# Kernel tuning notes

Measured on AMD Instinct MI355X. Metric: run time of the kernel, lower is better.

The kernel has to match this reference:

```python
import jax, jax.numpy as jnp
import numpy as np

INPUT_DIM = 1024
OUTPUT_DIM = 1024
DEGREE = 8


def setup_inputs() -> dict:
    key = jax.random.key(0)
    k1, k2 = jax.random.split(key)
    x = jax.random.normal(k1, (8192, INPUT_DIM), dtype=jnp.float32)
    std = 1.0 / (INPUT_DIM * (DEGREE + 1))
    cheby_coeffs = jax.random.normal(k2, (INPUT_DIM, OUTPUT_DIM, DEGREE + 1), dtype=jnp.float32) * std
    return {"x": x, "cheby_coeffs": cheby_coeffs}


def reference(x, cheby_coeffs):
    # x: [B, I]; cheby_coeffs: [I, O, D+1]
    degree = cheby_coeffs.shape[-1] - 1
    t = jnp.clip(jnp.tanh(x), -0.999, 0.999)            # [B, I]
    theta = jnp.arccos(t)[..., None]                     # [B, I, 1]
    arange = jnp.arange(degree + 1, dtype=x.dtype)       # [D+1]
    basis = jnp.cos(theta * arange)                      # [B, I, D+1] Chebyshev T_d(t)
    y = jnp.einsum('bid,iod->bo', basis, cheby_coeffs)   # [B, O]
    return y
```

## Files before the change

kernel.cpp:

```cpp
#include <hip/hip_runtime.h>
#include <stdint.h>

#define B_ROWS 8192
#define I_DIM  1024
#define N_DIM  1024
#define NDEG   9
#define K_DIM  (I_DIM * (NDEG-1))

#define BM 256
#define BN 128
#define BK 64
#define NT (K_DIM / BK)

typedef __attribute__((ext_vector_type(8)))  short short8;
typedef __attribute__((ext_vector_type(16))) float f32x16;

__device__ __forceinline__ unsigned short f2bf(float f) {
  union { float f; uint32_t u; } v; v.f = f;
  uint32_t u = v.u;
  u += 0x7FFFu + ((u >> 16) & 1u);
  return (unsigned short)(u >> 16);
}

__device__ __forceinline__ float bf2f(unsigned short h) {
  union { uint32_t u; float f; } v; v.u = ((uint32_t)h) << 16;
  return v.f;
}

__device__ __forceinline__ uint32_t pk_bf16(float lo, float hi) {
  uint32_t r;
  asm("v_cvt_pk_bf16_f32 %0, %1, %2" : "=v"(r) : "v"(lo), "v"(hi));
  return r;
}

__device__ __forceinline__ float fast_tanh(float x) {
  float e = __expf(2.0f * x);
  return 1.0f - __fdividef(2.0f, e + 1.0f);
}

__global__ __launch_bounds__(256) void repack_kernel(const float* __restrict__ cf,
                                                     unsigned short* __restrict__ Bt2,
                                                     float* __restrict__ bias) {
  __shared__ unsigned short L[32][584];
  const int i0  = blockIdx.x * 32;
  const int o0  = blockIdx.y * 64;
  const int tid = threadIdx.x;

  #pragma unroll
  for (int j = 0; j < 18; ++j) {
    const int f4  = j * 256 + tid;
    const int il  = f4 / 144;
    const int odq = f4 % 144;
    const float4 v = *reinterpret_cast<const float4*>(
        cf + ((size_t)(i0 + il) * N_DIM + o0) * NDEG + (size_t)odq * 4);
    ushort4 w;
    w.x = f2bf(v.x); w.y = f2bf(v.y); w.z = f2bf(v.z); w.w = f2bf(v.w);
    *reinterpret_cast<ushort4*>(&L[il][odq * 4]) = w;
  }
  __syncthreads();

  const int o_rel = tid >> 2;
  const int ci    = tid & 3;
  const int o     = o0 + o_rel;
  const int ntb   = o >> 7;
  const int gb    = (o & 127) >> 5;
  const int r31   = o & 31;
  const int kti   = (i0 >> 3) + ci;
  const size_t base = (size_t)ntb * 1048576 + (size_t)kti * 8192 + (size_t)r31 * 8;
  #pragma unroll
  for (int p = 0; p < 8; ++p) {
    const int il = ci * 8 + p;
    uint4 u;
    u.x = (uint32_t)L[il][o_rel*9 + 1] | ((uint32_t)L[il][o_rel*9 + 2] << 16);
    u.y = (uint32_t)L[il][o_rel*9 + 3] | ((uint32_t)L[il][o_rel*9 + 4] << 16);
    u.z = (uint32_t)L[il][o_rel*9 + 5] | ((uint32_t)L[il][o_rel*9 + 6] << 16);
    u.w = (uint32_t)L[il][o_rel*9 + 7] | ((uint32_t)L[il][o_rel*9 + 8] << 16);
    *reinterpret_cast<uint4*>(Bt2 + base + (size_t)(gb * 8 + p) * 256) = u;
  }
  if (tid < 64) {
    float s = 0.f;
    #pragma unroll
    for (int il = 0; il < 32; ++il) s += bf2f(L[il][tid * 9]);
    atomicAdd(&bias[o0 + tid], s);
  }
}

__global__ __launch_bounds__(768, 3) void gemm_kernel(const float* __restrict__ x,
                                                      const unsigned short* __restrict__ Bt2,
                                                      const float* __restrict__ bias,
                                                      float* __restrict__ C) {
  extern __shared__ unsigned short sm[];
  const int tid  = threadIdx.x;
  const int wave = tid >> 6;

  const int bid = blockIdx.x;
  const int mt  = (bid & 7) + 8 * (bid >> 6);
  const int nt  = (bid >> 3) & 7;
  const int m0  = mt * BM;
  const int n0  = nt * BN;

  if (wave < 8) {
    const int lane = tid & 63;
    const int l31  = lane & 31;
    const int half = lane >> 5;
    const int wm   = wave >> 1;
    const int wn   = wave & 1;

    const int aoff0 = ((wm * 2 + 0) * 8 + half) * 256 + l31 * 8;
    const int aoff1 = ((wm * 2 + 1) * 8 + half) * 256 + l31 * 8;
    const int boff0 = ((wn * 2 + 0) * 8 + half) * 256 + l31 * 8;
    const int boff1 = ((wn * 2 + 1) * 8 + half) * 256 + l31 * 8;

    f32x16 acc[2][2];
    #pragma unroll
    for (int a = 0; a < 2; ++a)
      #pragma unroll
      for (int b = 0; b < 2; ++b)
        #pragma unroll
        for (int r = 0; r < 16; ++r)
          acc[a][b][r] = 0.f;

    short8 av[2][4], bv[2][4];

#define READ4(As_, Bs_, ks) {                                                                \
    av[0][ks] = *reinterpret_cast<const short8*>(&(As_)[aoff0 + (ks) * 512]);                \
    av[1][ks] = *reinterpret_cast<const short8*>(&(As_)[aoff1 + (ks) * 512]);                \
    bv[0][ks] = *reinterpret_cast<const short8*>(&(Bs_)[boff0 + (ks) * 512]);                \
    bv[1][ks] = *reinterpret_cast<const short8*>(&(Bs_)[boff1 + (ks) * 512]); }

#define MFMA4(ks)                                                                            \
    acc[0][0] = __builtin_amdgcn_mfma_f32_32x32x16_bf16(av[0][ks], bv[0][ks], acc[0][0], 0, 0, 0); \
    acc[0][1] = __builtin_amdgcn_mfma_f32_32x32x16_bf16(av[0][ks], bv[1][ks], acc[0][1], 0, 0, 0); \
    acc[1][0] = __builtin_amdgcn_mfma_f32_32x32x16_bf16(av[1][ks], bv[0][ks], acc[1][0], 0, 0, 0); \
    acc[1][1] = __builtin_amdgcn_mfma_f32_32x32x16_bf16(av[1][ks], bv[1][ks], acc[1][1], 0, 0, 0);

#define CPIN { __builtin_amdgcn_sched_group_barrier(0x100, 4, 0);                            \
               __builtin_amdgcn_sched_group_barrier(0x008, 4, 0); }

#define CTILE(bufsel) {                                                                      \
    const unsigned short* As_ = &sm[(bufsel) * 16384];                                       \
    const unsigned short* Bs_ = &sm[32768 + (bufsel) * 8192];                                \
    READ4(As_, Bs_, 0)                                                                       \
    READ4(As_, Bs_, 1) MFMA4(0) CPIN                                                         \
    READ4(As_, Bs_, 2) MFMA4(1) CPIN                                                         \
    READ4(As_, Bs_, 3) MFMA4(2) CPIN                                                         \
    MFMA4(3) __builtin_amdgcn_sched_group_barrier(0x008, 4, 0); }

#define CBAR { __builtin_amdgcn_sched_barrier(0); __builtin_amdgcn_s_barrier();              \
               __builtin_amdgcn_sched_barrier(0); }

    CBAR
    for (int kt = 0; kt < 126; kt += 2) {
      CTILE(0) CBAR
      CTILE(1) CBAR
    }
    CTILE(0) CBAR
    CTILE(1)
#undef CTILE
#undef CPIN
#undef READ4

    #pragma unroll
    for (int ni = 0; ni < 2; ++ni) {
      const int col  = n0 + wn * 64 + ni * 32 + l31;
      const float bc = bias[col];
      #pragma unroll
      for (int mi = 0; mi < 2; ++mi) {
        const int rbase = m0 + wm * 64 + mi * 32 + 4 * half;
        #pragma unroll
        for (int r = 0; r < 16; ++r) {
          const int row = rbase + (r & 3) + 8 * (r >> 2);
          C[(size_t)row * N_DIM + col] = acc[mi][ni][r] + bc;
        }
      }
    }
#undef MFMA4
#undef CBAR
  } else {
    const int pr = tid - 512;
    const float* xrow = x + (size_t)(m0 + pr) * I_DIM;
    const unsigned short* BtSlab = Bt2 + (size_t)nt * 1048576;
    const int awbase = (pr >> 5) * 2048 + (pr & 31) * 8;
    const int prw8   = pr * 8;

#define STAGEB(bufsel, kt1) {                                                                \
    _Pragma("unroll")                                                                        \
    for (int q = 0; q < 4; ++q) {                                                            \
      __builtin_amdgcn_global_load_lds(                                                      \
        (const __attribute__((address_space(1))) void*)(BtSlab + (size_t)(kt1) * 8192 + q * 2048 + prw8), \
        (__attribute__((address_space(3))) void*)&sm[32768 + (bufsel) * 8192 + q * 2048 + prw8], 16, 0, 0); \
    } }

#define BASIS8(bufsel, f0, f1) {                                                             \
    const float tin[8] = {(f0).x, (f0).y, (f0).z, (f0).w, (f1).x, (f1).y, (f1).z, (f1).w};   \
    _Pragma("unroll")                                                                        \
    for (int s = 0; s < 8; ++s) {                                                            \
      float t = fast_tanh(tin[s]);                                                           \
      t = fminf(fmaxf(t, -0.999f), 0.999f);                                                  \
      const float t2 = t + t;                                                                \
      const float T1 = t;                                                                    \
      const float T2 = t2 * t - 1.0f;                                                        \
      const float T3 = t2 * T2 - T1;                                                         \
      const float T4 = t2 * T3 - T2;                                                         \
      const float T5 = t2 * T4 - T3;                                                         \
      const float T6 = t2 * T5 - T4;                                                         \
      const float T7 = t2 * T6 - T5;                                                         \
      const float T8 = t2 * T7 - T6;                                                         \
      uint4 u;                                                                               \
      u.x = pk_bf16(T1, T2); u.y = pk_bf16(T3, T4);                                          \
      u.z = pk_bf16(T5, T6); u.w = pk_bf16(T7, T8);                                          \
      *reinterpret_cast<uint4*>(&sm[(bufsel) * 16384 + awbase + s * 256]) = u;               \
    } }

    float4 xE0, xE1, xO0, xO1;
    xE0 = *reinterpret_cast<const float4*>(xrow + 0);
    xE1 = *reinterpret_cast<const float4*>(xrow + 4);
    xO0 = *reinterpret_cast<const float4*>(xrow + 8);
    xO1 = *reinterpret_cast<const float4*>(xrow + 12);
    STAGEB(0, 0)
    BASIS8(0, xE0, xE1)
    __builtin_amdgcn_sched_barrier(0);
    asm volatile("s_waitcnt vmcnt(0) lgkmcnt(0)" ::: "memory");
    __builtin_amdgcn_s_barrier();
    __builtin_amdgcn_sched_barrier(0);

#define PTILE(kt_, XU0, XU1, XL0, XL1, LX) {                                                 \
    STAGEB(((kt_) + 1) & 1, (kt_) + 1)                                                       \
    __builtin_amdgcn_sched_barrier(0);                                                       \
    BASIS8(((kt_) + 1) & 1, XU0, XU1)                                                        \
    __builtin_amdgcn_sched_barrier(0);                                                       \
    if (LX) {                                                                                \
      XL0 = *reinterpret_cast<const float4*>(xrow + ((kt_) + 2) * 8);                        \
      XL1 = *reinterpret_cast<const float4*>(xrow + ((kt_) + 2) * 8 + 4);                    \
    }                                                                                        \
    __builtin_amdgcn_sched_barrier(0);                                                       \
    if (LX) { asm volatile("s_waitcnt vmcnt(2) lgkmcnt(0)" ::: "memory"); }                  \
    else    { asm volatile("s_waitcnt vmcnt(0) lgkmcnt(0)" ::: "memory"); }                  \
    __builtin_amdgcn_s_barrier();                                                            \
    __builtin_amdgcn_sched_barrier(0); }

    for (int kt = 0; kt < 126; kt += 2) {
      PTILE(kt,     xO0, xO1, xE0, xE1, 1)
      PTILE(kt + 1, xE0, xE1, xO0, xO1, 1)
    }
    PTILE(126, xO0, xO1, xE0, xE1, 0)
#undef PTILE
#undef BASIS8
#undef STAGEB
  }
}

extern "C" void kernel_launch(void* const* d_in, const int* in_sizes, int n_in,
                              void* d_out, int out_size, void* d_ws, size_t ws_size,
                              hipStream_t stream) {
  const float* x      = (const float*)d_in[0];
  const float* coeffs = (const float*)d_in[1];
  float* y            = (float*)d_out;

  const size_t bt_bytes = (size_t)N_DIM * K_DIM * sizeof(unsigned short);
  unsigned short* Bt2 = (unsigned short*)d_ws;
  float* bias         = (float*)((char*)d_ws + bt_bytes);

  hipMemsetAsync(bias, 0, N_DIM * sizeof(float), stream);

  hipFuncSetAttribute((const void*)gemm_kernel,
                      hipFuncAttributeMaxDynamicSharedMemorySize, 98304);

  repack_kernel<<<dim3(I_DIM / 32, N_DIM / 64), 256, 0, stream>>>(coeffs, Bt2, bias);
  gemm_kernel<<<(B_ROWS / BM) * (N_DIM / BN), 768, 98304, stream>>>(x, Bt2, bias, y);
}
```

Baseline: 266.3 us.

## Drop LDS staging; compute basis and load B directly into registers per wave

Removes the producer-wave specialization and shared-memory double buffering. Each MFMA wave now loads its own x scalars and B fragments straight from global memory into registers, computes the Chebyshev basis in registers and feeds the MFMAs, with software double-buffered register prefetch. This eliminates LDS traffic and block barriers, but each wave recomputes the basis for its rows (2x redundancy across wn) and issues scattered scalar and vector global loads that rely on cache for reuse.

```diff
diff --git a/kernel.cpp b/kernel.cpp
--- a/kernel.cpp
+++ b/kernel.cpp
@@ -85,13 +85,17 @@
   }
 }
 
-__global__ __launch_bounds__(768, 3) void gemm_kernel(const float* __restrict__ x,
-                                                      const unsigned short* __restrict__ Bt2,
-                                                      const float* __restrict__ bias,
-                                                      float* __restrict__ C) {
-  extern __shared__ unsigned short sm[];
+__global__ __launch_bounds__(512) void gemm_kernel(const float* __restrict__ x,
+                                                   const unsigned short* __restrict__ Bt2,
+                                                   const float* __restrict__ bias,
+                                                   float* __restrict__ C) {
   const int tid  = threadIdx.x;
+  const int lane = tid & 63;
   const int wave = tid >> 6;
+  const int l31  = lane & 31;
+  const int half = lane >> 5;
+  const int wm   = wave >> 1;
+  const int wn   = wave & 1;
 
   const int bid = blockIdx.x;
   const int mt  = (bid & 7) + 8 * (bid >> 6);
@@ -99,154 +103,95 @@
   const int m0  = mt * BM;
   const int n0  = nt * BN;
 
-  if (wave < 8) {
-    const int lane = tid & 63;
-    const int l31  = lane & 31;
-    const int half = lane >> 5;
-    const int wm   = wave >> 1;
-    const int wn   = wave & 1;
-
-    const int aoff0 = ((wm * 2 + 0) * 8 + half) * 256 + l31 * 8;
-    const int aoff1 = ((wm * 2 + 1) * 8 + half) * 256 + l31 * 8;
-    const int boff0 = ((wn * 2 + 0) * 8 + half) * 256 + l31 * 8;
-    const int boff1 = ((wn * 2 + 1) * 8 + half) * 256 + l31 * 8;
-
-    f32x16 acc[2][2];
+  const float* xb = x + (size_t)(m0 + wm * 64 + l31) * I_DIM + half;
+  const unsigned short* bf = Bt2 + (size_t)nt * 1048576 + (size_t)(wn * 16 + half) * 256 + l31 * 8;
+
+  f32x16 acc[2][2];
+  #pragma unroll
+  for (int a = 0; a < 2; ++a)
     #pragma unroll
-    for (int a = 0; a < 2; ++a)
+    for (int b = 0; b < 2; ++b)
       #pragma unroll
-      for (int b = 0; b < 2; ++b)
-        #pragma unroll
-        for (int r = 0; r < 16; ++r)
-          acc[a][b][r] = 0.f;
-
-    short8 av[2][4], bv[2][4];
-
-#define READ4(As_, Bs_, ks) {                                                                \
-    av[0][ks] = *reinterpret_cast<const short8*>(&(As_)[aoff0 + (ks) * 512]);                \
-    av[1][ks] = *reinterpret_cast<const short8*>(&(As_)[aoff1 + (ks) * 512]);                \
-    bv[0][ks] = *reinterpret_cast<const short8*>(&(Bs_)[boff0 + (ks) * 512]);                \
-    bv[1][ks] = *reinterpret_cast<const short8*>(&(Bs_)[boff1 + (ks) * 512]); }
-
-#define MFMA4(ks)                                                                            \
-    acc[0][0] = __builtin_amdgcn_mfma_f32_32x32x16_bf16(av[0][ks], bv[0][ks], acc[0][0], 0, 0, 0); \
-    acc[0][1] = __builtin_amdgcn_mfma_f32_32x32x16_bf16(av[0][ks], bv[1][ks], acc[0][1], 0, 0, 0); \
-    acc[1][0] = __builtin_amdgcn_mfma_f32_32x32x16_bf16(av[1][ks], bv[0][ks], acc[1][0], 0, 0, 0); \
-    acc[1][1] = __builtin_amdgcn_mfma_f32_32x32x16_bf16(av[1][ks], bv[1][ks], acc[1][1], 0, 0, 0);
-
-#define CPIN { __builtin_amdgcn_sched_group_barrier(0x100, 4, 0);                            \
-               __builtin_amdgcn_sched_group_barrier(0x008, 4, 0); }
-
-#define CTILE(bufsel) {                                                                      \
-    const unsigned short* As_ = &sm[(bufsel) * 16384];                                       \
-    const unsigned short* Bs_ = &sm[32768 + (bufsel) * 8192];                                \
-    READ4(As_, Bs_, 0)                                                                       \
-    READ4(As_, Bs_, 1) MFMA4(0) CPIN                                                         \
-    READ4(As_, Bs_, 2) MFMA4(1) CPIN                                                         \
-    READ4(As_, Bs_, 3) MFMA4(2) CPIN                                                         \
-    MFMA4(3) __builtin_amdgcn_sched_group_barrier(0x008, 4, 0); }
-
-#define CBAR { __builtin_amdgcn_sched_barrier(0); __builtin_amdgcn_s_barrier();              \
-               __builtin_amdgcn_sched_barrier(0); }
-
-    CBAR
-    for (int kt = 0; kt < 126; kt += 2) {
-      CTILE(0) CBAR
-      CTILE(1) CBAR
-    }
-    CTILE(0) CBAR
-    CTILE(1)
-#undef CTILE
-#undef CPIN
-#undef READ4
-
+      for (int r = 0; r < 16; ++r)
+        acc[a][b][r] = 0.f;
+
+#define LOADT(TS, kt_) {                                                                     \
+    _Pragma("unroll")                                                                        \
+    for (int mi = 0; mi < 2; ++mi)                                                           \
+      _Pragma("unroll")                                                                      \
+      for (int ks = 0; ks < 4; ++ks)                                                         \
+        TS[mi][ks] = xb[(size_t)mi * 32 * I_DIM + (kt_) * 8 + ks * 2]; }
+
+#define LOADB(BV, kt_) {                                                                     \
+    _Pragma("unroll")                                                                        \
+    for (int ni = 0; ni < 2; ++ni)                                                           \
+      _Pragma("unroll")                                                                      \
+      for (int ks = 0; ks < 4; ++ks)                                                         \
+        BV[ni][ks] = *reinterpret_cast<const short8*>(                                       \
+            bf + (size_t)(kt_) * 8192 + (ni * 8 + ks * 2) * 256); }
+
+#define BASIS(AV, TS) {                                                                      \
+    _Pragma("unroll")                                                                        \
+    for (int mi = 0; mi < 2; ++mi)                                                           \
+      _Pragma("unroll")                                                                      \
+      for (int ks = 0; ks < 4; ++ks) {                                                       \
+        float t = fast_tanh(TS[mi][ks]);                                                     \
+        t = fminf(fmaxf(t, -0.999f), 0.999f);                                                \
+        const float t2 = t + t;                                                              \
+        const float T1 = t;                                                                  \
+        const float T2 = t2 * t - 1.0f;                                                      \
+        const float T3 = t2 * T2 - T1;                                                       \
+        const float T4 = t2 * T3 - T2;                                                       \
+        const float T5 = t2 * T4 - T3;                                                       \
+        const float T6 = t2 * T5 - T4;                                                       \
+        const float T7 = t2 * T6 - T5;                                                       \
+        const float T8 = t2 * T7 - T6;                                                       \
+        union { uint4 u; short8 s; } p;                                                      \
+        p.u.x = pk_bf16(T1, T2); p.u.y = pk_bf16(T3, T4);                                    \
+        p.u.z = pk_bf16(T5, T6); p.u.w = pk_bf16(T7, T8);                                    \
+        AV[mi][ks] = p.s; } }
+
+#define MFMA16(AV, BV) {                                                                     \
+    _Pragma("unroll")                                                                        \
+    for (int ks = 0; ks < 4; ++ks) {                                                         \
+      acc[0][0] = __builtin_amdgcn_mfma_f32_32x32x16_bf16(AV[0][ks], BV[0][ks], acc[0][0], 0, 0, 0); \
+      acc[0][1] = __builtin_amdgcn_mfma_f32_32x32x16_bf16(AV[0][ks], BV[1][ks], acc[0][1], 0, 0, 0); \
+      acc[1][0] = __builtin_amdgcn_mfma_f32_32x32x16_bf16(AV[1][ks], BV[0][ks], acc[1][0], 0, 0, 0); \
+      acc[1][1] = __builtin_amdgcn_mfma_f32_32x32x16_bf16(AV[1][ks], BV[1][ks], acc[1][1], 0, 0, 0); } }
+
+  float  tsA[2][4], tsB[2][4];
+  short8 bvA[2][4], bvB[2][4], av[2][4];
+
+  LOADT(tsA, 0) LOADB(bvA, 0)
+  for (int kt = 0; kt < 126; kt += 2) {
+    LOADT(tsB, kt + 1) LOADB(bvB, kt + 1)
+    BASIS(av, tsA)
+    MFMA16(av, bvA)
+    LOADT(tsA, kt + 2) LOADB(bvA, kt + 2)
+    BASIS(av, tsB)
+    MFMA16(av, bvB)
+  }
+  LOADT(tsB, 127) LOADB(bvB, 127)
+  BASIS(av, tsA) MFMA16(av, bvA)
+  BASIS(av, tsB) MFMA16(av, bvB)
+#undef MFMA16
+#undef BASIS
+#undef LOADB
+#undef LOADT
+
+  #pragma unroll
+  for (int ni = 0; ni < 2; ++ni) {
+    const int col  = n0 + wn * 64 + ni * 32 + l31;
+    const float bc = bias[col];
     #pragma unroll
-    for (int ni = 0; ni < 2; ++ni) {
-      const int col  = n0 + wn * 64 + ni * 32 + l31;
-      const float bc = bias[col];
+    for (int mi = 0; mi < 2; ++mi) {
+      const int rbase = m0 + wm * 64 + mi * 32 + 4 * half;
       #pragma unroll
-      for (int mi = 0; mi < 2; ++mi) {
-        const int rbase = m0 + wm * 64 + mi * 32 + 4 * half;
-        #pragma unroll
-        for (int r = 0; r < 16; ++r) {
-          const int row = rbase + (r & 3) + 8 * (r >> 2);
-          C[(size_t)row * N_DIM + col] = acc[mi][ni][r] + bc;
-        }
+      for (int r = 0; r < 16; ++r) {
+        const int row = rbase + (r & 3) + 8 * (r >> 2);
+        C[(size_t)row * N_DIM + col] = acc[mi][ni][r] + bc;
       }
     }
-#undef MFMA4
-#undef CBAR
-  } else {
-    const int pr = tid - 512;
-    const float* xrow = x + (size_t)(m0 + pr) * I_DIM;
-    const unsigned short* BtSlab = Bt2 + (size_t)nt * 1048576;
-    const int awbase = (pr >> 5) * 2048 + (pr & 31) * 8;
-    const int prw8   = pr * 8;
-
-#define STAGEB(bufsel, kt1) {                                                                \
-    _Pragma("unroll")                                                                        \
-    for (int q = 0; q < 4; ++q) {                                                            \
-      __builtin_amdgcn_global_load_lds(                                                      \
-        (const __attribute__((address_space(1))) void*)(BtSlab + (size_t)(kt1) * 8192 + q * 2048 + prw8), \
-        (__attribute__((address_space(3))) void*)&sm[32768 + (bufsel) * 8192 + q * 2048 + prw8], 16, 0, 0); \
-    } }
-
-#define BASIS8(bufsel, f0, f1) {                                                             \
-    const float tin[8] = {(f0).x, (f0).y, (f0).z, (f0).w, (f1).x, (f1).y, (f1).z, (f1).w};   \
-    _Pragma("unroll")                                                                        \
-    for (int s = 0; s < 8; ++s) {                                                            \
-      float t = fast_tanh(tin[s]);                                                           \
-      t = fminf(fmaxf(t, -0.999f), 0.999f);                                                  \
-      const float t2 = t + t;                                                                \
-      const float T1 = t;                                                                    \
-      const float T2 = t2 * t - 1.0f;                                                        \
-      const float T3 = t2 * T2 - T1;                                                         \
-      const float T4 = t2 * T3 - T2;                                                         \
-      const float T5 = t2 * T4 - T3;                                                         \
-      const float T6 = t2 * T5 - T4;                                                         \
-      const float T7 = t2 * T6 - T5;                                                         \
-      const float T8 = t2 * T7 - T6;                                                         \
-      uint4 u;                                                                               \
-      u.x = pk_bf16(T1, T2); u.y = pk_bf16(T3, T4);                                          \
-      u.z = pk_bf16(T5, T6); u.w = pk_bf16(T7, T8);                                          \
-      *reinterpret_cast<uint4*>(&sm[(bufsel) * 16384 + awbase + s * 256]) = u;               \
-    } }
-
-    float4 xE0, xE1, xO0, xO1;
-    xE0 = *reinterpret_cast<const float4*>(xrow + 0);
-    xE1 = *reinterpret_cast<const float4*>(xrow + 4);
-    xO0 = *reinterpret_cast<const float4*>(xrow + 8);
-    xO1 = *reinterpret_cast<const float4*>(xrow + 12);
-    STAGEB(0, 0)
-    BASIS8(0, xE0, xE1)
-    __builtin_amdgcn_sched_barrier(0);
-    asm volatile("s_waitcnt vmcnt(0) lgkmcnt(0)" ::: "memory");
-    __builtin_amdgcn_s_barrier();
-    __builtin_amdgcn_sched_barrier(0);
-
-#define PTILE(kt_, XU0, XU1, XL0, XL1, LX) {                                                 \
-    STAGEB(((kt_) + 1) & 1, (kt_) + 1)                                                       \
-    __builtin_amdgcn_sched_barrier(0);                                                       \
-    BASIS8(((kt_) + 1) & 1, XU0, XU1)                                                        \
-    __builtin_amdgcn_sched_barrier(0);                                                       \
-    if (LX) {                                                                                \
-      XL0 = *reinterpret_cast<const float4*>(xrow + ((kt_) + 2) * 8);                        \
-      XL1 = *reinterpret_cast<const float4*>(xrow + ((kt_) + 2) * 8 + 4);                    \
-    }                                                                                        \
-    __builtin_amdgcn_sched_barrier(0);                                                       \
-    if (LX) { asm volatile("s_waitcnt vmcnt(2) lgkmcnt(0)" ::: "memory"); }                  \
-    else    { asm volatile("s_waitcnt vmcnt(0) lgkmcnt(0)" ::: "memory"); }                  \
-    __builtin_amdgcn_s_barrier();                                                            \
-    __builtin_amdgcn_sched_barrier(0); }
-
-    for (int kt = 0; kt < 126; kt += 2) {
-      PTILE(kt,     xO0, xO1, xE0, xE1, 1)
-      PTILE(kt + 1, xE0, xE1, xO0, xO1, 1)
-    }
-    PTILE(126, xO0, xO1, xE0, xE1, 0)
-#undef PTILE
-#undef BASIS8
-#undef STAGEB
   }
 }
 
@@ -263,9 +208,7 @@
 
   hipMemsetAsync(bias, 0, N_DIM * sizeof(float), stream);
 
-  hipFuncSetAttribute((const void*)gemm_kernel,
-                      hipFuncAttributeMaxDynamicSharedMemorySize, 98304);
-
   repack_kernel<<<dim3(I_DIM / 32, N_DIM / 64), 256, 0, stream>>>(coeffs, Bt2, bias);
-  gemm_kernel<<<(B_ROWS / BM) * (N_DIM / BN), 768, 98304, stream>>>(x, Bt2, bias, y);
-}
+
+  gemm_kernel<<<(B_ROWS / BM) * (N_DIM / BN), 512, 0, stream>>>(x, Bt2, bias, y);
+}
```

Measured after the change: 401.2 us. 1.51x slower.
